# Kernel tuning notes

Hardware: AMD Instinct MI355X
Metric: run time of the kernel (lower is better)

## Reference

```python
import jax, jax.numpy as jnp
import numpy as np

H = 768
NH = 12
HD = H // NH
FF = 3072
E = 4
EPS = 1e-12


def _make_expert_params(key):
    ks = jax.random.split(key, 8)
    s = 0.02
    return {
        'wq': jax.random.normal(ks[0], (H, H), jnp.float32) * s,
        'wk': jax.random.normal(ks[1], (H, H), jnp.float32) * s,
        'wv': jax.random.normal(ks[2], (H, H), jnp.float32) * s,
        'wo': jax.random.normal(ks[3], (H, H), jnp.float32) * s,
        'bq': jnp.zeros((H,), jnp.float32),
        'bk': jnp.zeros((H,), jnp.float32),
        'bv': jnp.zeros((H,), jnp.float32),
        'bo': jnp.zeros((H,), jnp.float32),
        'ln1_g': jnp.ones((H,), jnp.float32),
        'ln1_b': jnp.zeros((H,), jnp.float32),
        'w1': jax.random.normal(ks[4], (H, FF), jnp.float32) * s,
        'b1': jnp.zeros((FF,), jnp.float32),
        'w2': jax.random.normal(ks[5], (FF, H), jnp.float32) * s,
        'b2': jnp.zeros((H,), jnp.float32),
        'ln2_g': jnp.ones((H,), jnp.float32),
        'ln2_b': jnp.zeros((H,), jnp.float32),
    }


def setup_inputs() -> dict:
    key = jax.random.key(0)
    k1, k2, kp = jax.random.split(key, 3)
    hidden_states = jax.random.normal(k1, (64, 128, H), jnp.float32)
    attention_mask = jnp.zeros((64, 128), jnp.float32)  # additive mask, 0 = attend
    centers = jax.random.normal(k2, (E, H), jnp.float32)
    pkeys = jax.random.split(kp, E)
    ps = [_make_expert_params(k) for k in pkeys]
    # stack expert params along leading axis for vectorized gather-by-expert
    params = {k: jnp.stack([p[k] for p in ps], axis=0) for k in ps[0]}
    out = {'hidden_states': hidden_states, 'attention_mask': attention_mask, 'centers': centers}
    out.update(params)
    return out


def _layernorm(x, g, b):
    mu = x.mean(-1, keepdims=True)
    var = ((x - mu) ** 2).mean(-1, keepdims=True)
    return (x - mu) * jax.lax.rsqrt(var + EPS) * g + b


def _encoder(x, mask, p):
    # x: [B,S,H], mask: [B,S] additive; p: per-sample expert params (leading dim B)
    B, S, _ = x.shape
    q = jnp.einsum('bsh,bhd->bsd', x, p['wq']) + p['bq'][:, None, :]
    k = jnp.einsum('bsh,bhd->bsd', x, p['wk']) + p['bk'][:, None, :]
    v = jnp.einsum('bsh,bhd->bsd', x, p['wv']) + p['bv'][:, None, :]
    q = q.reshape(B, S, NH, HD)
    k = k.reshape(B, S, NH, HD)
    v = v.reshape(B, S, NH, HD)
    scores = jnp.einsum('bqnd,bknd->bnqk', q, k) / np.sqrt(HD).astype(np.float32)
    scores = scores + mask[:, None, None, :]
    attn = jax.nn.softmax(scores, axis=-1)
    ctx = jnp.einsum('bnqk,bknd->bqnd', attn, v).reshape(B, S, H)
    att_out = jnp.einsum('bsh,bhd->bsd', ctx, p['wo']) + p['bo'][:, None, :]
    att_out = _layernorm(att_out + x, p['ln1_g'][:, None, :], p['ln1_b'][:, None, :])
    ffn = jnp.einsum('bsh,bhf->bsf', att_out, p['w1']) + p['b1'][:, None, :]
    ffn = jax.nn.gelu(ffn)
    ffn = jnp.einsum('bsf,bfh->bsh', ffn, p['w2']) + p['b2'][:, None, :]
    out = _layernorm(att_out + ffn, p['ln2_g'][:, None, :], p['ln2_b'][:, None, :])
    return out


def reference(hidden_states, attention_mask, centers,
              wq, wk, wv, wo, bq, bk, bv, bo, ln1_g, ln1_b,
              w1, b1, w2, b2, ln2_g, ln2_b):
    # routing: mean over seq, cdist to centers, argmin -> per-sentence expert id
    h_pca = hidden_states.mean(axis=1)  # [B,H]
    d2 = (jnp.sum(h_pca ** 2, -1, keepdims=True)
          - 2.0 * h_pca @ centers.T
          + jnp.sum(centers ** 2, -1)[None, :])
    eid = jnp.argmin(d2, axis=1)  # [B]
    params = {'wq': wq, 'wk': wk, 'wv': wv, 'wo': wo, 'bq': bq, 'bk': bk,
              'bv': bv, 'bo': bo, 'ln1_g': ln1_g, 'ln1_b': ln1_b,
              'w1': w1, 'b1': b1, 'w2': w2, 'b2': b2,
              'ln2_g': ln2_g, 'ln2_b': ln2_b}
    # gather per-sample expert params (jit-friendly, honors hard routing)
    psel = {k: v[eid] for k, v in params.items()}
    return _encoder(hidden_states, attention_mask, psel)
```

## Files before the change

kernel.cpp:

```cpp
#include <hip/hip_runtime.h>
#include <hip/hip_bf16.h>
#include <math.h>

#define HDIM 768
#define NHEAD 12
#define HEADD 64
#define FFDIM 3072
#define NEXP 4
#define SEQ 128
#define NB 64
#define QKVN 2304

typedef __attribute__((ext_vector_type(8))) _Float16 f16x8;
typedef __attribute__((ext_vector_type(4))) _Float16 f16x4;
typedef __attribute__((ext_vector_type(4))) float f32x4;

__device__ __forceinline__ float gelu_fast(float x) {
  float t = -1.5957691216057308f * x * __builtin_fmaf(0.044715f * x, x, 1.0f);
  return x * __builtin_amdgcn_rcpf(1.0f + __expf(t));
}

__device__ __forceinline__ void gld_lds16(const void* g, void* l) {
  __builtin_amdgcn_global_load_lds(
      (const __attribute__((address_space(1))) unsigned int*)g,
      (__attribute__((address_space(3))) unsigned int*)l, 16, 0, 0);
}

__global__ __launch_bounds__(256) void route_cvt_kernel(
    const float* __restrict__ hs, const float* __restrict__ centers,
    int* __restrict__ eid, _Float16* __restrict__ x16) {
  int b = blockIdx.x, t = threadIdx.x;
  __shared__ float hp[HDIM];
  __shared__ float dist[NEXP];
  const float* xb = hs + (size_t)b * SEQ * HDIM;
  _Float16* ob = x16 + (size_t)b * SEQ * HDIM;

  if (t < 192) {
    float p0 = 0.f, p1 = 0.f, p2 = 0.f, p3 = 0.f;
    for (int sq = 0; sq < SEQ; ++sq) {
      float4 v = ((const float4*)(xb + (size_t)sq * HDIM))[t];
      p0 += v.x; p1 += v.y; p2 += v.z; p3 += v.w;
      f16x4 h = {(_Float16)v.x, (_Float16)v.y, (_Float16)v.z, (_Float16)v.w};
      *(f16x4*)(ob + (size_t)sq * HDIM + t * 4) = h;
    }
    hp[t * 4 + 0] = p0 * (1.0f / SEQ);
    hp[t * 4 + 1] = p1 * (1.0f / SEQ);
    hp[t * 4 + 2] = p2 * (1.0f / SEQ);
    hp[t * 4 + 3] = p3 * (1.0f / SEQ);
  }
  if (t < NEXP) dist[t] = 0.f;
  __syncthreads();

  float pe[NEXP] = {0.f, 0.f, 0.f, 0.f};
  for (int h = t; h < HDIM; h += 256) {
    float v = hp[h];
#pragma unroll
    for (int e = 0; e < NEXP; ++e) {
      float d = v - centers[e * HDIM + h];
      pe[e] += d * d;
    }
  }
#pragma unroll
  for (int e = 0; e < NEXP; ++e) atomicAdd(&dist[e], pe[e]);
  __syncthreads();
  if (t == 0) {
    int best = 0; float bv = dist[0];
    for (int e = 1; e < NEXP; ++e) if (dist[e] < bv) { bv = dist[e]; best = e; }
    eid[b] = best;
  }
}

__device__ __forceinline__ void tr_tile(const float* __restrict__ ip,
                                        _Float16* __restrict__ op,
                                        int K, int N, int nb, int kb,
                                        float (*tile)[33], int t) {
  int tx = t & 31, ty = t >> 5;
  for (int i = ty; i < 32; i += 8)
    tile[i][tx] = ip[(size_t)(kb + i) * N + nb + tx];
  __syncthreads();
  for (int i = ty; i < 32; i += 8)
    op[(size_t)(nb + i) * K + kb + tx] = (_Float16)tile[tx][i];
}

__global__ __launch_bounds__(256) void prep_weights(
    const float* __restrict__ wq, const float* __restrict__ wk,
    const float* __restrict__ wv, const float* __restrict__ wo,
    const float* __restrict__ w1, const float* __restrict__ w2,
    const float* __restrict__ bq, const float* __restrict__ bk,
    const float* __restrict__ bv,
    _Float16* __restrict__ Wqkvt, _Float16* __restrict__ Wot,
    _Float16* __restrict__ W1t, _Float16* __restrict__ W2t,
    float* __restrict__ bqkv, const int* __restrict__ eid,
    int* __restrict__ order, int* __restrict__ ord_eid) {
  __shared__ float tile[32][33];
  int x = blockIdx.x, e = blockIdx.y, t = threadIdx.x;

  if (x < 1728) {
    int which = x / 576, local = x % 576;
    const float* src = (which == 0) ? wq : (which == 1) ? wk : wv;
    tr_tile(src + (size_t)e * HDIM * HDIM,
            Wqkvt + (size_t)which * HDIM * HDIM + (size_t)e * QKVN * HDIM,
            HDIM, HDIM, (local % 24) * 32, (local / 24) * 32, tile, t);
  } else if (x < 2304) {
    int local = x - 1728;
    tr_tile(wo + (size_t)e * HDIM * HDIM, Wot + (size_t)e * HDIM * HDIM,
            HDIM, HDIM, (local % 24) * 32, (local / 24) * 32, tile, t);
  } else if (x < 4608) {
    int local = x - 2304;
    tr_tile(w1 + (size_t)e * HDIM * FFDIM, W1t + (size_t)e * FFDIM * HDIM,
            HDIM, FFDIM, (local % 96) * 32, (local / 96) * 32, tile, t);
  } else if (x < 6912) {
    int local = x - 4608;
    tr_tile(w2 + (size_t)e * FFDIM * HDIM, W2t + (size_t)e * HDIM * FFDIM,
            FFDIM, HDIM, (local % 24) * 32, (local / 24) * 32, tile, t);
  } else if (x < 6948) {
    if (e == 0) {
      int i = (x - 6912) * 256 + t;
      if (i < NEXP * QKVN) {
        int ee = i / QKVN, n = i % QKVN;
        float v = (n < HDIM) ? bq[ee * HDIM + n]
                : (n < 2 * HDIM) ? bk[ee * HDIM + n - HDIM]
                                 : bv[ee * HDIM + n - 2 * HDIM];
        bqkv[i] = v;
      }
    }
  } else {
    if (e == 0 && t == 0) {
      int n = 0;
      for (int ee = 0; ee < NEXP; ++ee)
        for (int b = 0; b < NB; ++b)
          if (eid[b] == ee) { order[n] = b; ord_eid[n] = ee; n++; }
    }
  }
}

template <int OUT_F16, int GELU, int KDIM, int SPLITK>
__global__ __launch_bounds__(256) void gemm_mfma(
    const _Float16* __restrict__ A, const _Float16* __restrict__ Wt,
    const float* __restrict__ Ball, const int* __restrict__ order,
    const int* __restrict__ ord_eid, void* __restrict__ Cv, int N) {
  constexpr int K = KDIM;
  constexpr int Kp = KDIM / SPLITK;
  constexpr int NIT = Kp / 32;
  int GX = N >> 7;
  int L = blockIdx.x;
  int low3 = L & 7, Mq = L >> 3;
  int x = Mq % GX, zhi = Mq / GX;
  int z = zhi * 8 + low3;
  int b = order[z];
  int e = ord_eid[z];
  int col0 = x * 128;
  int kz = blockIdx.y;
  int kbeg = kz * Kp;

  int t = threadIdx.x;
  int lane = t & 63, w = t >> 6;
  int quad = lane >> 4, l16 = lane & 15;
  int wr = (w >> 1) * 64, wc = (w & 1) * 64;

  __shared__ __align__(16) _Float16 As[3 * 128 * 32];
  __shared__ __align__(16) _Float16 Bs[3 * 128 * 32];

  const _Float16* Ab = A + (size_t)b * SEQ * K + kbeg;
  const _Float16* Wb = Wt + (size_t)e * N * K + (size_t)col0 * K + kbeg;

  int e0 = t * 8, e1 = 2048 + t * 8;
  int m0 = e0 >> 5, k0e = e0 & 31;
  int m1 = e1 >> 5, k1e = e1 & 31;
  const _Float16* ga0 = Ab + (size_t)m0 * K + k0e;
  const _Float16* ga1 = Ab + (size_t)m1 * K + k1e;
  const _Float16* gb0 = Wb + (size_t)m0 * K + k0e;
  const _Float16* gb1 = Wb + (size_t)m1 * K + k1e;

  auto issue = [&](int c, int st) {
    int off = c * 32;
    _Float16* Ast = As + st * 4096;
    _Float16* Bst = Bs + st * 4096;
    gld_lds16(ga0 + off, Ast + e0);
    gld_lds16(ga1 + off, Ast + e1);
    gld_lds16(gb0 + off, Bst + e0);
    gld_lds16(gb1 + off, Bst + e1);
  };

  f32x4 acc[4][4];
#pragma unroll
  for (int i = 0; i < 4; ++i)
#pragma unroll
    for (int j = 0; j < 4; ++j) acc[i][j] = (f32x4){0.f, 0.f, 0.f, 0.f};

  issue(0, 0);
  if (NIT > 1) issue(1, 1);

#pragma unroll
  for (int it = 0; it < NIT; ++it) {
    if (it < NIT - 1) __builtin_amdgcn_s_waitcnt(0xF74);
    else              __builtin_amdgcn_s_waitcnt(0xF70);
    __builtin_amdgcn_s_barrier();

    int st = it % 3;
    const _Float16* Ast = As + st * 4096;
    const _Float16* Bst = Bs + st * 4096;
    f16x8 af[4], bf[4];
#pragma unroll
    for (int i = 0; i < 4; ++i)
      af[i] = *(const f16x8*)&Ast[(wr + i * 16 + l16) * 32 + quad * 8];
#pragma unroll
    for (int i = 0; i < 4; ++i)
      bf[i] = *(const f16x8*)&Bst[(wc + i * 16 + l16) * 32 + quad * 8];
#pragma unroll
    for (int i = 0; i < 4; ++i)
#pragma unroll
      for (int j = 0; j < 4; ++j)
        acc[i][j] = __builtin_amdgcn_mfma_f32_16x16x32_f16(af[i], bf[j], acc[i][j], 0, 0, 0);

    if (it + 2 < NIT) issue(it + 2, (it + 2) % 3);
  }

  const float* bias = Ball + (size_t)e * N;

  if (OUT_F16) {
    _Float16* Ch = (_Float16*)Cv + (size_t)b * SEQ * N;
#pragma unroll
    for (int i = 0; i < 4; ++i)
#pragma unroll
      for (int j = 0; j < 4; ++j) {
        int col = col0 + wc + j * 16 + l16;
        float bv = bias[col];
#pragma unroll
        for (int r = 0; r < 4; ++r) {
          int row = wr + i * 16 + quad * 4 + r;
          float v = acc[i][j][r] + bv;
          if (GELU) v = gelu_fast(v);
          Ch[(size_t)row * N + col] = (_Float16)v;
        }
      }
  } else {
    float* Cf = (float*)Cv + (size_t)kz * NB * SEQ * N + (size_t)b * SEQ * N;
    float bscale = (kz == 0) ? 1.f : 0.f;
#pragma unroll
    for (int i = 0; i < 4; ++i)
#pragma unroll
      for (int j = 0; j < 4; ++j) {
        int col = col0 + wc + j * 16 + l16;
        float bv = bias[col] * bscale;
#pragma unroll
        for (int r = 0; r < 4; ++r) {
          int row = wr + i * 16 + quad * 4 + r;
          Cf[(size_t)row * N + col] = acc[i][j][r] + bv;
        }
      }
  }
}

__global__ __launch_bounds__(256) void attn_mfma(
    const _Float16* __restrict__ QKV, const float* __restrict__ mask,
    _Float16* __restrict__ Ctx) {
  int h = blockIdx.x, b = blockIdx.y;
  int t = threadIdx.x;
  int w = t >> 6, lane = t & 63, quad = lane >> 4, l16 = lane & 15;

  __shared__ __align__(16) char smem[54784];
  _Float16* Qs = (_Float16*)smem;
  _Float16* Ks = (_Float16*)(smem + 18432);
  _Float16* Ps = (_Float16*)smem;
  _Float16* Vt = (_Float16*)(smem + 36864);
  float* mrow = (float*)(smem + 54272);

  const _Float16* Qb = QKV + (size_t)b * SEQ * QKVN + h * HEADD;
  const _Float16* Kb = Qb + HDIM;
  const _Float16* Vb = Qb + 2 * HDIM;

#pragma unroll
  for (int it = 0; it < 4; ++it) {
    int chunk = t + it * 256;
    int row = chunk >> 3, c = chunk & 7;
    *(f16x8*)&Qs[row * 72 + c * 8] = *(const f16x8*)(Qb + (size_t)row * QKVN + c * 8);
    *(f16x8*)&Ks[row * 72 + c * 8] = *(const f16x8*)(Kb + (size_t)row * QKVN + c * 8);
  }
  {
    int vc = t & 7, vjp0 = t >> 3;
#pragma unroll
    for (int it = 0; it < 2; ++it) {
      int jp = vjp0 + it * 32;
      f16x8 v0 = *(const f16x8*)(Vb + (size_t)(2 * jp) * QKVN + vc * 8);
      f16x8 v1 = *(const f16x8*)(Vb + (size_t)(2 * jp + 1) * QKVN + vc * 8);
#pragma unroll
      for (int i = 0; i < 8; ++i) {
        int d = vc * 8 + i;
        unsigned ua = __builtin_bit_cast(unsigned short, (_Float16)v0[i]);
        unsigned ub = __builtin_bit_cast(unsigned short, (_Float16)v1[i]);
        ((unsigned*)Vt)[d * 68 + jp] = ua | (ub << 16);
      }
    }
  }
  if (t < SEQ) mrow[t] = mask[(size_t)b * SEQ + t];
  __syncthreads();

  int m0 = w * 32;
  f32x4 accs[2][8];
#pragma unroll
  for (int i = 0; i < 2; ++i)
#pragma unroll
    for (int j = 0; j < 8; ++j) accs[i][j] = (f32x4){0.f, 0.f, 0.f, 0.f};

#pragma unroll
  for (int ks = 0; ks < 2; ++ks) {
    int k0 = ks * 32 + quad * 8;
    f16x8 af[2], bf[8];
#pragma unroll
    for (int i = 0; i < 2; ++i)
      af[i] = *(const f16x8*)&Qs[(m0 + i * 16 + l16) * 72 + k0];
#pragma unroll
    for (int j = 0; j < 8; ++j)
      bf[j] = *(const f16x8*)&Ks[(j * 16 + l16) * 72 + k0];
#pragma unroll
    for (int i = 0; i < 2; ++i)
#pragma unroll
      for (int j = 0; j < 8; ++j)
        accs[i][j] = __builtin_amdgcn_mfma_f32_16x16x32_f16(af[i], bf[j], accs[i][j], 0, 0, 0);
  }
  __syncthreads();

  float mv[8];
#pragma unroll
  for (int j = 0; j < 8; ++j) mv[j] = mrow[j * 16 + l16];

  float linv[2][4];
#pragma unroll
  for (int i = 0; i < 2; ++i) {
#pragma unroll
    for (int j = 0; j < 8; ++j)
#pragma unroll
      for (int r = 0; r < 4; ++r)
        accs[i][j][r] = accs[i][j][r] * 0.125f + mv[j];
#pragma unroll
    for (int r = 0; r < 4; ++r) {
      float m = accs[i][0][r];
#pragma unroll
      for (int j = 1; j < 8; ++j) m = fmaxf(m, accs[i][j][r]);
      m = fmaxf(m, __shfl_xor(m, 1));
      m = fmaxf(m, __shfl_xor(m, 2));
      m = fmaxf(m, __shfl_xor(m, 4));
      m = fmaxf(m, __shfl_xor(m, 8));
      float sum = 0.f;
#pragma unroll
      for (int j = 0; j < 8; ++j) {
        float p = __expf(accs[i][j][r] - m);
        accs[i][j][r] = p;
        sum += p;
      }
      sum += __shfl_xor(sum, 1);
      sum += __shfl_xor(sum, 2);
      sum += __shfl_xor(sum, 4);
      sum += __shfl_xor(sum, 8);
      linv[i][r] = 1.f / sum;
    }
    int rowb = m0 + i * 16 + quad * 4;
#pragma unroll
    for (int j = 0; j < 8; ++j)
#pragma unroll
      for (int r = 0; r < 4; ++r)
        Ps[(rowb + r) * 136 + j * 16 + l16] = (_Float16)accs[i][j][r];
  }
  __syncthreads();

  f32x4 acco[2][4];
#pragma unroll
  for (int i = 0; i < 2; ++i)
#pragma unroll
    for (int j = 0; j < 4; ++j) acco[i][j] = (f32x4){0.f, 0.f, 0.f, 0.f};

#pragma unroll
  for (int ks = 0; ks < 4; ++ks) {
    int k0 = ks * 32 + quad * 8;
    f16x8 pa[2], vf[4];
#pragma unroll
    for (int i = 0; i < 2; ++i)
      pa[i] = *(const f16x8*)&Ps[(m0 + i * 16 + l16) * 136 + k0];
#pragma unroll
    for (int j = 0; j < 4; ++j)
      vf[j] = *(const f16x8*)&Vt[(j * 16 + l16) * 136 + k0];
#pragma unroll
    for (int i = 0; i < 2; ++i)
#pragma unroll
      for (int j = 0; j < 4; ++j)
        acco[i][j] = __builtin_amdgcn_mfma_f32_16x16x32_f16(pa[i], vf[j], acco[i][j], 0, 0, 0);
  }

  _Float16* Cb = Ctx + (size_t)b * SEQ * HDIM + h * HEADD;
#pragma unroll
  for (int i = 0; i < 2; ++i)
#pragma unroll
    for (int j = 0; j < 4; ++j)
#pragma unroll
      for (int r = 0; r < 4; ++r) {
        int row = m0 + i * 16 + quad * 4 + r;
        int d = j * 16 + l16;
        Cb[(size_t)row * HDIM + d] = (_Float16)(acco[i][j][r] * linv[i][r]);
      }
}

template <int NP>
__global__ __launch_bounds__(256) void resid_ln_kernel(
    const float* __restrict__ X, const float* __restrict__ P0,
    const float* __restrict__ P1,
    const float* __restrict__ Gall, const float* __restrict__ Ball,
    const int* __restrict__ eid, float* __restrict__ Out,
    _Float16* __restrict__ Out16) {
  int row = blockIdx.x, b = blockIdx.y, t = threadIdx.x;
  int e = eid[b];
  size_t off = ((size_t)b * SEQ + row) * HDIM;
  const float* x = X + off;
  const float* p0 = P0 + off;
  const float* p1 = (NP > 1) ? P1 + off : nullptr;
  float* o = Out + off;
  const float* g = Gall + (size_t)e * HDIM;
  const float* bb = Ball + (size_t)e * HDIM;

  __shared__ float buf[HDIM];
  __shared__ float red[256];

  float s = 0.f;
  for (int h = t; h < HDIM; h += 256) {
    float v = x[h] + p0[h];
    if (NP > 1) v += p1[h];
    buf[h] = v;
    s += v;
  }
  red[t] = s;
  __syncthreads();
  for (int off2 = 128; off2 > 0; off2 >>= 1) {
    if (t < off2) red[t] += red[t + off2];
    __syncthreads();
  }
  float mean = red[0] * (1.0f / HDIM);
  __syncthreads();

  float s2 = 0.f;
  for (int h = t; h < HDIM; h += 256) {
    float d = buf[h] - mean;
    s2 += d * d;
  }
  red[t] = s2;
  __syncthreads();
  for (int off2 = 128; off2 > 0; off2 >>= 1) {
    if (t < off2) red[t] += red[t + off2];
    __syncthreads();
  }
  float var = red[0] * (1.0f / HDIM);
  float rs = rsqrtf(var + 1e-12f);

  for (int h = t; h < HDIM; h += 256) {
    float v = (buf[h] - mean) * rs * g[h] + bb[h];
    o[h] = v;
    if (Out16) Out16[off + h] = (_Float16)v;
  }
}

extern "C" void kernel_launch(void* const* d_in, const int* in_sizes, int n_in,
                              void* d_out, int out_size, void* d_ws, size_t ws_size,
                              hipStream_t stream) {
  const float* hs   = (const float*)d_in[0];
  const float* mask = (const float*)d_in[1];
  const float* cen  = (const float*)d_in[2];
  const float* wq = (const float*)d_in[3];
  const float* wk = (const float*)d_in[4];
  const float* wv = (const float*)d_in[5];
  const float* wo = (const float*)d_in[6];
  const float* bq = (const float*)d_in[7];
  const float* bk = (const float*)d_in[8];
  const float* bv = (const float*)d_in[9];
  const float* bo = (const float*)d_in[10];
  const float* ln1g = (const float*)d_in[11];
  const float* ln1b = (const float*)d_in[12];
  const float* w1 = (const float*)d_in[13];
  const float* b1 = (const float*)d_in[14];
  const float* w2 = (const float*)d_in[15];
  const float* b2 = (const float*)d_in[16];
  const float* ln2g = (const float*)d_in[17];
  const float* ln2b = (const float*)d_in[18];
  float* out = (float*)d_out;

  const size_t sh = (size_t)SEQ * HDIM;

  char* p = (char*)d_ws;
  int* eid = (int*)p;                 p += 256;
  int* order = (int*)p;               p += 256;
  int* ord_eid = (int*)p;             p += 256;
  float* bqkv = (float*)p;            p += (size_t)NEXP * QKVN * 4;
  _Float16* Wqkvt = (_Float16*)p;     p += (size_t)NEXP * QKVN * HDIM * 2;
  _Float16* Wot = (_Float16*)p;       p += (size_t)NEXP * HDIM * HDIM * 2;
  _Float16* W1t = (_Float16*)p;       p += (size_t)NEXP * FFDIM * HDIM * 2;
  _Float16* W2t = (_Float16*)p;       p += (size_t)NEXP * HDIM * FFDIM * 2;
  _Float16* x16 = (_Float16*)p;       p += (size_t)NB * sh * 2;

  char* region = p;                   p += (size_t)NB * SEQ * QKVN * 2;
  _Float16* ctx16 = (_Float16*)p;     p += (size_t)NB * sh * 2;
  float* aof = (float*)p;             p += (size_t)NB * sh * 4;
  _Float16* ao16 = (_Float16*)p;      p += (size_t)NB * sh * 2;
  char* ffreg = p;                    p += (size_t)NB * SEQ * FFDIM * 2;

  float* woparts = (float*)ffreg;
  float* w2parts = (float*)region;
  _Float16* ff16 = (_Float16*)ffreg;

  route_cvt_kernel<<<NB, 256, 0, stream>>>(hs, cen, eid, x16);
  prep_weights<<<dim3(6949, NEXP), 256, 0, stream>>>(
      wq, wk, wv, wo, w1, w2, bq, bk, bv,
      Wqkvt, Wot, W1t, W2t, bqkv, eid, order, ord_eid);
  gemm_mfma<1, 0, HDIM, 1><<<dim3((QKVN / 128) * NB, 1), 256, 0, stream>>>(
      x16, Wqkvt, bqkv, order, ord_eid, region, QKVN);
  attn_mfma<<<dim3(NHEAD, NB), 256, 0, stream>>>(
      (const _Float16*)region, mask, ctx16);
  gemm_mfma<0, 0, HDIM, 2><<<dim3((HDIM / 128) * NB, 2), 256, 0, stream>>>(
      ctx16, Wot, bo, order, ord_eid, woparts, HDIM);
  resid_ln_kernel<2><<<dim3(SEQ, NB), 256, 0, stream>>>(
      hs, woparts, woparts + (size_t)NB * sh, ln1g, ln1b, eid, aof, ao16);
  gemm_mfma<1, 1, HDIM, 1><<<dim3((FFDIM / 128) * NB, 1), 256, 0, stream>>>(
      ao16, W1t, b1, order, ord_eid, ff16, FFDIM);
  gemm_mfma<0, 0, FFDIM, 2><<<dim3((HDIM / 128) * NB, 2), 256, 0, stream>>>(
      ff16, W2t, b2, order, ord_eid, w2parts, HDIM);
  resid_ln_kernel<2><<<dim3(SEQ, NB), 256, 0, stream>>>(
      aof, w2parts, w2parts + (size_t)NB * sh, ln2g, ln2b, eid, out,
      (_Float16*)nullptr);
}
```

Baseline: 467.5 us.

## Add XOR-swizzled LDS layout and wide 128x256 GEMM tile for QKV and FFN1

Loads into LDS now use an XOR swizzle on the k-quarter index so the MFMA fragment reads avoid bank conflicts. A new gemm_wide kernel uses a 128x256 output tile with double buffering and replaces the 128x128 kernel for the QKV and FFN-up projections. Each A tile is then reused across twice as many output columns, which halves A traffic and the block count. The cost is 128 accumulator registers per thread, which lowers occupancy, and an extra barrier per k-step.

```diff
diff --git a/kernel.cpp b/kernel.cpp
--- a/kernel.cpp
+++ b/kernel.cpp
@@ -134,6 +134,7 @@
   }
 }
 
+
 template <int OUT_F16, int GELU, int KDIM, int SPLITK>
 __global__ __launch_bounds__(256) void gemm_mfma(
     const _Float16* __restrict__ A, const _Float16* __restrict__ Wt,
@@ -158,29 +159,31 @@
   int quad = lane >> 4, l16 = lane & 15;
   int wr = (w >> 1) * 64, wc = (w & 1) * 64;
 
-  __shared__ __align__(16) _Float16 As[3 * 128 * 32];
-  __shared__ __align__(16) _Float16 Bs[3 * 128 * 32];
+  __shared__ __align__(16) _Float16 As[3 * 4096];
+  __shared__ __align__(16) _Float16 Bs[3 * 4096];
 
   const _Float16* Ab = A + (size_t)b * SEQ * K + kbeg;
   const _Float16* Wb = Wt + (size_t)e * N * K + (size_t)col0 * K + kbeg;
 
-  int e0 = t * 8, e1 = 2048 + t * 8;
-  int m0 = e0 >> 5, k0e = e0 & 31;
-  int m1 = e1 >> 5, k1e = e1 & 31;
-  const _Float16* ga0 = Ab + (size_t)m0 * K + k0e;
-  const _Float16* ga1 = Ab + (size_t)m1 * K + k1e;
-  const _Float16* gb0 = Wb + (size_t)m0 * K + k0e;
-  const _Float16* gb1 = Wb + (size_t)m1 * K + k1e;
+  int mg = t >> 2, sl = t & 3;
+  int kq = sl ^ (mg & 3) ^ ((mg >> 2) & 3);
+  const _Float16* ga0 = Ab + (size_t)mg * K + kq * 8;
+  const _Float16* ga1 = Ab + (size_t)(64 + mg) * K + kq * 8;
+  const _Float16* gb0 = Wb + (size_t)mg * K + kq * 8;
+  const _Float16* gb1 = Wb + (size_t)(64 + mg) * K + kq * 8;
+  int e0 = t * 8;
 
   auto issue = [&](int c, int st) {
     int off = c * 32;
     _Float16* Ast = As + st * 4096;
     _Float16* Bst = Bs + st * 4096;
     gld_lds16(ga0 + off, Ast + e0);
-    gld_lds16(ga1 + off, Ast + e1);
+    gld_lds16(ga1 + off, Ast + 2048 + e0);
     gld_lds16(gb0 + off, Bst + e0);
-    gld_lds16(gb1 + off, Bst + e1);
+    gld_lds16(gb1 + off, Bst + 2048 + e0);
   };
+
+  int koff = (quad ^ (l16 & 3) ^ ((l16 >> 2) & 3)) * 8;
 
   f32x4 acc[4][4];
 #pragma unroll
@@ -203,10 +206,10 @@
     f16x8 af[4], bf[4];
 #pragma unroll
     for (int i = 0; i < 4; ++i)
-      af[i] = *(const f16x8*)&Ast[(wr + i * 16 + l16) * 32 + quad * 8];
+      af[i] = *(const f16x8*)&Ast[(wr + i * 16 + l16) * 32 + koff];
 #pragma unroll
     for (int i = 0; i < 4; ++i)
-      bf[i] = *(const f16x8*)&Bst[(wc + i * 16 + l16) * 32 + quad * 8];
+      bf[i] = *(const f16x8*)&Bst[(wc + i * 16 + l16) * 32 + koff];
 #pragma unroll
     for (int i = 0; i < 4; ++i)
 #pragma unroll
@@ -250,6 +253,111 @@
         }
       }
   }
+}
+
+template <int GELU, int KDIM>
+__global__ __launch_bounds__(256) void gemm_wide(
+    const _Float16* __restrict__ A, const _Float16* __restrict__ Wt,
+    const float* __restrict__ Ball, const int* __restrict__ order,
+    const int* __restrict__ ord_eid, _Float16* __restrict__ Cv, int N) {
+  constexpr int K = KDIM;
+  constexpr int NIT = KDIM / 32;
+  int GX = N >> 8;
+  int L = blockIdx.x;
+  int low3 = L & 7, Mq = L >> 3;
+  int x = Mq % GX, zhi = Mq / GX;
+  int z = zhi * 8 + low3;
+  int b = order[z];
+  int e = ord_eid[z];
+  int col0 = x * 256;
+
+  int t = threadIdx.x;
+  int lane = t & 63, w = t >> 6;
+  int quad = lane >> 4, l16 = lane & 15;
+  int wr = (w >> 1) * 64, wc = (w & 1) * 128;
+
+  __shared__ __align__(16) _Float16 As[2 * 4096];
+  __shared__ __align__(16) _Float16 Bs[2 * 8192];
+
+  const _Float16* Ab = A + (size_t)b * SEQ * K;
+  const _Float16* Wb = Wt + (size_t)e * N * K + (size_t)col0 * K;
+
+  int mg = t >> 2, sl = t & 3;
+  int kq = sl ^ (mg & 3) ^ ((mg >> 2) & 3);
+  const _Float16* ga0 = Ab + (size_t)mg * K + kq * 8;
+  const _Float16* ga1 = Ab + (size_t)(64 + mg) * K + kq * 8;
+  const _Float16* gb0 = Wb + (size_t)mg * K + kq * 8;
+  const _Float16* gb1 = Wb + (size_t)(64 + mg) * K + kq * 8;
+  const _Float16* gb2 = Wb + (size_t)(128 + mg) * K + kq * 8;
+  const _Float16* gb3 = Wb + (size_t)(192 + mg) * K + kq * 8;
+  int e0 = t * 8;
+
+  auto issue = [&](int c, int st) {
+    int off = c * 32;
+    _Float16* Ast = As + st * 4096;
+    _Float16* Bst = Bs + st * 8192;
+    gld_lds16(ga0 + off, Ast + e0);
+    gld_lds16(ga1 + off, Ast + 2048 + e0);
+    gld_lds16(gb0 + off, Bst + e0);
+    gld_lds16(gb1 + off, Bst + 2048 + e0);
+    gld_lds16(gb2 + off, Bst + 4096 + e0);
+    gld_lds16(gb3 + off, Bst + 6144 + e0);
+  };
+
+  int koff = (quad ^ (l16 & 3) ^ ((l16 >> 2) & 3)) * 8;
+
+  f32x4 acc[4][8];
+#pragma unroll
+  for (int i = 0; i < 4; ++i)
+#pragma unroll
+    for (int j = 0; j < 8; ++j) acc[i][j] = (f32x4){0.f, 0.f, 0.f, 0.f};
+
+  issue(0, 0);
+
+#pragma unroll
+  for (int it = 0; it < NIT; ++it) {
+    if (it + 1 < NIT) {
+      issue(it + 1, (it + 1) & 1);
+      __builtin_amdgcn_s_waitcnt(0xF76);
+    } else {
+      __builtin_amdgcn_s_waitcnt(0xF70);
+    }
+    __builtin_amdgcn_s_barrier();
+
+    const _Float16* Ast = As + (it & 1) * 4096;
+    const _Float16* Bst = Bs + (it & 1) * 8192;
+    f16x8 af[4], bf[8];
+#pragma unroll
+    for (int i = 0; i < 4; ++i)
+      af[i] = *(const f16x8*)&Ast[(wr + i * 16 + l16) * 32 + koff];
+#pragma unroll
+    for (int j = 0; j < 8; ++j)
+      bf[j] = *(const f16x8*)&Bst[(wc + j * 16 + l16) * 32 + koff];
+#pragma unroll
+    for (int i = 0; i < 4; ++i)
+#pragma unroll
+      for (int j = 0; j < 8; ++j)
+        acc[i][j] = __builtin_amdgcn_mfma_f32_16x16x32_f16(af[i], bf[j], acc[i][j], 0, 0, 0);
+
+    __builtin_amdgcn_s_barrier();
+  }
+
+  const float* bias = Ball + (size_t)e * N;
+  _Float16* Ch = Cv + (size_t)b * SEQ * N;
+#pragma unroll
+  for (int i = 0; i < 4; ++i)
+#pragma unroll
+    for (int j = 0; j < 8; ++j) {
+      int col = col0 + wc + j * 16 + l16;
+      float bv = bias[col];
+#pragma unroll
+      for (int r = 0; r < 4; ++r) {
+        int row = wr + i * 16 + quad * 4 + r;
+        float v = acc[i][j][r] + bv;
+        if (GELU) v = gelu_fast(v);
+        Ch[(size_t)row * N + col] = (_Float16)v;
+      }
+    }
 }
 
 __global__ __launch_bounds__(256) void attn_mfma(
@@ -508,15 +616,15 @@
   prep_weights<<<dim3(6949, NEXP), 256, 0, stream>>>(
       wq, wk, wv, wo, w1, w2, bq, bk, bv,
       Wqkvt, Wot, W1t, W2t, bqkv, eid, order, ord_eid);
-  gemm_mfma<1, 0, HDIM, 1><<<dim3((QKVN / 128) * NB, 1), 256, 0, stream>>>(
-      x16, Wqkvt, bqkv, order, ord_eid, region, QKVN);
+  gemm_wide<0, HDIM><<<dim3((QKVN / 256) * NB, 1), 256, 0, stream>>>(
+      x16, Wqkvt, bqkv, order, ord_eid, (_Float16*)region, QKVN);
   attn_mfma<<<dim3(NHEAD, NB), 256, 0, stream>>>(
       (const _Float16*)region, mask, ctx16);
   gemm_mfma<0, 0, HDIM, 2><<<dim3((HDIM / 128) * NB, 2), 256, 0, stream>>>(
       ctx16, Wot, bo, order, ord_eid, woparts, HDIM);
   resid_ln_kernel<2><<<dim3(SEQ, NB), 256, 0, stream>>>(
       hs, woparts, woparts + (size_t)NB * sh, ln1g, ln1b, eid, aof, ao16);
-  gemm_mfma<1, 1, HDIM, 1><<<dim3((FFDIM / 128) * NB, 1), 256, 0, stream>>>(
+  gemm_wide<1, HDIM><<<dim3((FFDIM / 256) * NB, 1), 256, 0, stream>>>(
       ao16, W1t, b1, order, ord_eid, ff16, FFDIM);
   gemm_mfma<0, 0, FFDIM, 2><<<dim3((HDIM / 128) * NB, 2), 256, 0, stream>>>(
       ff16, W2t, b2, order, ord_eid, w2parts, HDIM);
```

Measured after the change: 534.6 us. +14.4%, slower.
